# Kernel optimization log

Hardware: AMD Instinct MI355X
Metric: run time of the kernel (lower is better)

The kernel has to match this reference:

```python
import jax, jax.numpy as jnp
import numpy as np

N, E, F_IN, H0, H1, H2 = 50000, 800000, 128, 256, 256, 256
NEG = jnp.finfo(jnp.float32).min


def sage_max(x, src, dst, Wl, bl, Wr):
    # PyG SAGEConv(aggr='max'): lin_l(max_j x_j) + lin_r(x_i)
    agg = jax.ops.segment_max(x[src], dst, num_segments=N)  # [N, F]
    agg = jnp.where(agg <= NEG, 0.0, agg)  # isolated nodes -> 0
    return agg @ Wl + bl + x @ Wr


def setup_inputs() -> dict:
    key = jax.random.key(0)
    ks = jax.random.split(key, 16)
    g = lambda k, shp, fan: jax.random.normal(k, shp, jnp.float32) / np.sqrt(fan)
    inp = {
        "x": jax.random.normal(ks[0], (N, F_IN), jnp.float32),
        "edge_index": jax.random.randint(ks[1], (2, E), 0, N, jnp.int64),
        # shared_l1
        "Wl1": g(ks[2], (F_IN, H0), F_IN), "bl1": jnp.zeros((H0,), jnp.float32), "Wr1": g(ks[3], (F_IN, H0), F_IN),
        # shared_l2
        "Wl2": g(ks[4], (H0, H1), H0), "bl2": jnp.zeros((H1,), jnp.float32), "Wr2": g(ks[5], (H0, H1), H0),
        # rtang_l1 + head
        "Wla": g(ks[6], (H1, H2), H1), "bla": jnp.zeros((H2,), jnp.float32), "Wra": g(ks[7], (H1, H2), H1),
        "Wa": g(ks[8], (H2, 1), H2), "ba": jnp.zeros((1,), jnp.float32),
        # movedis_l1 + head
        "Wlm": g(ks[9], (H1, H2), H1), "blm": jnp.zeros((H2,), jnp.float32), "Wrm": g(ks[10], (H1, H2), H1),
        "Wm": g(ks[11], (H2, 1), H2), "bm": jnp.zeros((1,), jnp.float32),
    }
    return inp


def reference(x, edge_index, Wl1, bl1, Wr1, Wl2, bl2, Wr2,
              Wla, bla, Wra, Wa, ba, Wlm, blm, Wrm, Wm, bm):
    src, dst = edge_index[0], edge_index[1]
    h = jax.nn.relu(sage_max(x, src, dst, Wl1, bl1, Wr1))
    h = jax.nn.relu(sage_max(h, src, dst, Wl2, bl2, Wr2))
    rt = jax.nn.relu(sage_max(h, src, dst, Wla, bla, Wra))
    rt = (rt @ Wa + ba).reshape(-1)  # [N]
    mv = jax.nn.relu(sage_max(h, src, dst, Wlm, blm, Wrm))
    mv = (mv @ Wm + bm).reshape(-1)  # [N]
    return (rt, mv)
```

## Files before the change

### kernel.cpp

```cpp
#include <hip/hip_runtime.h>
#include <hip/hip_bf16.h>


#define NN 50000
#define NE 800000
#define HD 256
#define CAP 64

using bf16 = __hip_bfloat16;
typedef float f32x4 __attribute__((ext_vector_type(4)));
typedef short bf16x8 __attribute__((ext_vector_type(8)));

__device__ __forceinline__ void async16(const void* g, void* l) {
    __builtin_amdgcn_global_load_lds(
        (const __attribute__((address_space(1))) unsigned int*)g,
        (__attribute__((address_space(3))) unsigned int*)l, 16, 0, 0);
}

__device__ __forceinline__ unsigned short f2b(float f) {
    bf16 b = __float2bfloat16(f);
    return __builtin_bit_cast(unsigned short, b);
}

__global__ void k_scatter(const int* __restrict__ ei, int* __restrict__ cnt,
                          int* __restrict__ srcp) {
    int e = blockIdx.x * 256 + threadIdx.x;
    if (e < NE) {
        int d = ei[NE + e];
        int slot = atomicAdd(&cnt[d], 1);
        if (slot < CAP) srcp[(d << 6) + slot] = ei[e];
    }
}

__device__ __forceinline__ void pack1(const float* __restrict__ W,
                                      bf16* __restrict__ bt, int idx, int Ktot,
                                      int kofs) {
    int k = idx >> 8, n = idx & 255;
    bt[(size_t)n * Ktot + kofs + k] = __float2bfloat16(W[idx]);
}

#define PREP_CVT_B 6250
#define PREP_PACK_B 1792
#define PREP_CNT_B 196
#define PREP_B (PREP_CVT_B + PREP_PACK_B + PREP_CNT_B)

__global__ void k_prep(const float* __restrict__ x, bf16* __restrict__ xb,
                       const float* __restrict__ Wl1,
                       const float* __restrict__ Wr1,
                       const float* __restrict__ Wl2,
                       const float* __restrict__ Wr2,
                       const float* __restrict__ Wla,
                       const float* __restrict__ Wra,
                       const float* __restrict__ Wlm,
                       const float* __restrict__ Wrm, bf16* __restrict__ Bt1,
                       bf16* __restrict__ Bt2, bf16* __restrict__ Bta,
                       bf16* __restrict__ Btm, int* __restrict__ cnt) {
    int b = blockIdx.x;
    if (b < PREP_CVT_B) {
        int i = b * 256 + threadIdx.x;
        float4 v = ((const float4*)x)[i];
        ushort4 o;
        o.x = f2b(v.x); o.y = f2b(v.y); o.z = f2b(v.z); o.w = f2b(v.w);
        ((ushort4*)xb)[i] = o;
    } else if (b < PREP_CVT_B + PREP_PACK_B) {
        int idx = (b - PREP_CVT_B) * 256 + threadIdx.x;
        if (idx < 32768) pack1(Wl1, Bt1, idx, 256, 0);
        else if (idx < 65536) pack1(Wr1, Bt1, idx - 32768, 256, 128);
        else if (idx < 131072) pack1(Wl2, Bt2, idx - 65536, 512, 0);
        else if (idx < 196608) pack1(Wr2, Bt2, idx - 131072, 512, 256);
        else if (idx < 262144) pack1(Wla, Bta, idx - 196608, 512, 0);
        else if (idx < 327680) pack1(Wra, Bta, idx - 262144, 512, 256);
        else if (idx < 393216) pack1(Wlm, Btm, idx - 327680, 512, 0);
        else pack1(Wrm, Btm, idx - 393216, 512, 256);
    } else {
        int i = (b - PREP_CVT_B - PREP_PACK_B) * 256 + threadIdx.x;
        if (i < NN) cnt[i] = 0;
    }
}

template <int EPL>
__global__ __launch_bounds__(256) void k_agg(const bf16* __restrict__ feat,
                                             bf16* __restrict__ agg,
                                             const int* __restrict__ cnt,
                                             const int* __restrict__ srcp) {
    int node = blockIdx.x * 4 + (threadIdx.x >> 6);
    if (node >= NN) return;
    int lane = threadIdx.x & 63;
    int n = min(cnt[node], CAP);
    const int* __restrict__ lst = srcp + (node << 6);
    float m[EPL];
#pragma unroll
    for (int i = 0; i < EPL; ++i) m[i] = __int_as_float(0xff800000);

    auto acc2 = [&](unsigned v, int i0) {
        m[i0] = fmaxf(m[i0], __uint_as_float(v << 16));
        m[i0 + 1] = fmaxf(m[i0 + 1], __uint_as_float(v & 0xffff0000u));
    };

    int e = 0;
    for (; e + 3 < n; e += 4) {
        int sa = lst[e], sb = lst[e + 1], sc = lst[e + 2], sd = lst[e + 3];
        if (EPL == 2) {
            unsigned va = ((const unsigned*)feat)[(size_t)sa * 64 + lane];
            unsigned vb = ((const unsigned*)feat)[(size_t)sb * 64 + lane];
            unsigned vc = ((const unsigned*)feat)[(size_t)sc * 64 + lane];
            unsigned vd = ((const unsigned*)feat)[(size_t)sd * 64 + lane];
            acc2(va, 0); acc2(vb, 0); acc2(vc, 0); acc2(vd, 0);
        } else {
            uint2 va = ((const uint2*)feat)[(size_t)sa * 64 + lane];
            uint2 vb = ((const uint2*)feat)[(size_t)sb * 64 + lane];
            uint2 vc = ((const uint2*)feat)[(size_t)sc * 64 + lane];
            uint2 vd = ((const uint2*)feat)[(size_t)sd * 64 + lane];
            acc2(va.x, 0); acc2(va.y, 2);
            acc2(vb.x, 0); acc2(vb.y, 2);
            acc2(vc.x, 0); acc2(vc.y, 2);
            acc2(vd.x, 0); acc2(vd.y, 2);
        }
    }
    for (; e < n; ++e) {
        int s = lst[e];
        if (EPL == 2) {
            acc2(((const unsigned*)feat)[(size_t)s * 64 + lane], 0);
        } else {
            uint2 v = ((const uint2*)feat)[(size_t)s * 64 + lane];
            acc2(v.x, 0); acc2(v.y, 2);
        }
    }
    unsigned r0 = 0, r1 = 0;
    if (n > 0) {
        r0 = (__float_as_uint(m[0]) >> 16) | (__float_as_uint(m[1]) & 0xffff0000u);
        if (EPL == 4)
            r1 = (__float_as_uint(m[2]) >> 16) | (__float_as_uint(m[3]) & 0xffff0000u);
    }
    if (EPL == 2) {
        ((unsigned*)agg)[(size_t)node * 64 + lane] = r0;
    } else {
        ((uint2*)agg)[(size_t)node * 64 + lane] = make_uint2(r0, r1);
    }
}

__device__ __forceinline__ void gemm_core256(const bf16* __restrict__ A0,
                                             const bf16* __restrict__ A1, int F,
                                             int Ktot,
                                             const bf16* __restrict__ Bt,
                                             int bm0, int t, short* As,
                                             short* Bs, f32x4 (&acc)[4][8]) {
    const int wave = t >> 6;
    const int lane = t & 63;
    const int q = lane >> 4;
    const int c = lane & 15;
    const int wr = (wave >> 1) * 64;
    const int wcl = (wave & 1) * 128;

    for (int k0 = 0; k0 < Ktot; k0 += 64) {
        const bf16* Asrc = (k0 < F) ? A0 : A1;
        const int kk = (k0 < F) ? k0 : k0 - F;
        __syncthreads();
#pragma unroll
        for (int it = 0; it < 4; ++it) {
            int chunk = it * 256 + t;
            int row = chunk >> 3, kc = chunk & 7;
            int kcg = kc ^ (row & 7);
            int grow = bm0 + row;
            if (grow > NN - 1) grow = NN - 1;
            async16(Asrc + (size_t)grow * F + kk + kcg * 8, &As[chunk * 8]);
        }
#pragma unroll
        for (int it = 0; it < 8; ++it) {
            int chunk = it * 256 + t;
            int row = chunk >> 3, kc = chunk & 7;
            int kcg = kc ^ (row & 7);
            async16(Bt + (size_t)row * Ktot + k0 + kcg * 8, &Bs[chunk * 8]);
        }
        __syncthreads();
#pragma unroll
        for (int ks = 0; ks < 2; ++ks) {
            bf16x8 af[4], bfr[8];
            int ch = (ks * 4 + q) ^ (c & 7);
#pragma unroll
            for (int i = 0; i < 4; ++i)
                af[i] = *(const bf16x8*)&As[(wr + i * 16 + c) * 64 + ch * 8];
#pragma unroll
            for (int j = 0; j < 8; ++j)
                bfr[j] = *(const bf16x8*)&Bs[(wcl + j * 16 + c) * 64 + ch * 8];
#pragma unroll
            for (int i = 0; i < 4; ++i)
#pragma unroll
                for (int j = 0; j < 8; ++j)
                    acc[i][j] = __builtin_amdgcn_mfma_f32_16x16x32_bf16(
                        af[i], bfr[j], acc[i][j], 0, 0, 0);
        }
    }
}

__global__ __launch_bounds__(256, 2) void k_gemm_h(
    const bf16* __restrict__ A0, const bf16* __restrict__ A1, int F, int Ktot,
    const bf16* __restrict__ Bt, const float* __restrict__ bias,
    bf16* __restrict__ Hout) {
    __shared__ __attribute__((aligned(16))) short As[128 * 64];
    __shared__ __attribute__((aligned(16))) short Bs[256 * 64];
    const int t = threadIdx.x;
    const int bm0 = blockIdx.x * 128;
    const int wave = t >> 6;
    const int lane = t & 63;
    const int q = lane >> 4;
    const int c = lane & 15;
    const int wr = (wave >> 1) * 64;
    const int wcl = (wave & 1) * 128;

    f32x4 acc[4][8];
#pragma unroll
    for (int i = 0; i < 4; ++i)
#pragma unroll
        for (int j = 0; j < 8; ++j) acc[i][j] = (f32x4){0.f, 0.f, 0.f, 0.f};
    gemm_core256(A0, A1, F, Ktot, Bt, bm0, t, As, Bs, acc);

    float bcol[8];
#pragma unroll
    for (int j = 0; j < 8; ++j) bcol[j] = bias[wcl + j * 16 + c];
#pragma unroll
    for (int i = 0; i < 4; ++i)
#pragma unroll
        for (int r = 0; r < 4; ++r) {
            int row = bm0 + wr + i * 16 + q * 4 + r;
            if (row < NN) {
#pragma unroll
                for (int j = 0; j < 8; ++j) {
                    int col = wcl + j * 16 + c;
                    float v = fmaxf(acc[i][j][r] + bcol[j], 0.f);
                    Hout[(size_t)row * HD + col] = __float2bfloat16(v);
                }
            }
        }
}

__global__ __launch_bounds__(256, 2) void k_gemm_heads(
    const bf16* __restrict__ A0, const bf16* __restrict__ A1,
    const bf16* __restrict__ Bta, const float* __restrict__ bla,
    const float* __restrict__ Wa, const float* __restrict__ ba,
    const bf16* __restrict__ Btm, const float* __restrict__ blm,
    const float* __restrict__ Wm, const float* __restrict__ bm,
    float* __restrict__ out) {
    __shared__ __attribute__((aligned(16))) short As[128 * 64];
    __shared__ __attribute__((aligned(16))) short Bs[256 * 64];
    const int t = threadIdx.x;
    const int bm0 = blockIdx.x * 128;
    const int z = blockIdx.y;
    const bf16* Bt = z ? Btm : Bta;
    const float* bias = z ? blm : bla;
    const float* Wh = z ? Wm : Wa;
    const float hb = z ? bm[0] : ba[0];
    float* outp = out + (size_t)z * NN;
    const int wave = t >> 6;
    const int lane = t & 63;
    const int q = lane >> 4;
    const int c = lane & 15;
    const int wr = (wave >> 1) * 64;
    const int wcl = (wave & 1) * 128;

    f32x4 acc[4][8];
#pragma unroll
    for (int i = 0; i < 4; ++i)
#pragma unroll
        for (int j = 0; j < 8; ++j) acc[i][j] = (f32x4){0.f, 0.f, 0.f, 0.f};
    gemm_core256(A0, A1, 256, 512, Bt, bm0, t, As, Bs, acc);

    float bcol[8], wcol[8];
#pragma unroll
    for (int j = 0; j < 8; ++j) {
        int col = wcl + j * 16 + c;
        bcol[j] = bias[col];
        wcol[j] = Wh[col];
    }
    float pr[4][4];
#pragma unroll
    for (int i = 0; i < 4; ++i)
#pragma unroll
        for (int r = 0; r < 4; ++r) {
            float p = 0.f;
#pragma unroll
            for (int j = 0; j < 8; ++j)
                p += fmaxf(acc[i][j][r] + bcol[j], 0.f) * wcol[j];
            p += __shfl_xor(p, 1, 64);
            p += __shfl_xor(p, 2, 64);
            p += __shfl_xor(p, 4, 64);
            p += __shfl_xor(p, 8, 64);
            pr[i][r] = p;
        }
    __syncthreads();
    float* red = (float*)As;
    if ((wave & 1) && c == 0) {
#pragma unroll
        for (int i = 0; i < 4; ++i)
#pragma unroll
            for (int r = 0; r < 4; ++r) red[wr + i * 16 + q * 4 + r] = pr[i][r];
    }
    __syncthreads();
    if (!(wave & 1) && c == 0) {
#pragma unroll
        for (int i = 0; i < 4; ++i)
#pragma unroll
            for (int r = 0; r < 4; ++r) {
                int lr = wr + i * 16 + q * 4 + r;
                int row = bm0 + lr;
                if (row < NN) outp[row] = pr[i][r] + red[lr] + hb;
            }
    }
}

extern "C" void kernel_launch(void* const* d_in, const int* in_sizes, int n_in,
                              void* d_out, int out_size, void* d_ws,
                              size_t ws_size, hipStream_t stream) {
    const float* x = (const float*)d_in[0];
    const int* ei = (const int*)d_in[1];
    const float* Wl1 = (const float*)d_in[2];
    const float* bl1 = (const float*)d_in[3];
    const float* Wr1 = (const float*)d_in[4];
    const float* Wl2 = (const float*)d_in[5];
    const float* bl2 = (const float*)d_in[6];
    const float* Wr2 = (const float*)d_in[7];
    const float* Wla = (const float*)d_in[8];
    const float* bla = (const float*)d_in[9];
    const float* Wra = (const float*)d_in[10];
    const float* Wa = (const float*)d_in[11];
    const float* ba = (const float*)d_in[12];
    const float* Wlm = (const float*)d_in[13];
    const float* blm = (const float*)d_in[14];
    const float* Wrm = (const float*)d_in[15];
    const float* Wm = (const float*)d_in[16];
    const float* bm = (const float*)d_in[17];
    float* out = (float*)d_out;

    char* ws = (char*)d_ws;
    size_t off = 0;
    auto alloc = [&](size_t b) {
        void* p = ws + off;
        off = (off + b + 255) & ~(size_t)255;
        return p;
    };
    int* srcp = (int*)alloc((size_t)NN * CAP * 4);
    int* cnt = (int*)alloc((size_t)NN * 4);
    bf16* xb = (bf16*)alloc((size_t)NN * 128 * 2);
    bf16* h1 = (bf16*)alloc((size_t)NN * 256 * 2);
    bf16* h2 = (bf16*)alloc((size_t)NN * 256 * 2);
    bf16* agg = (bf16*)alloc((size_t)NN * 256 * 2);
    bf16* Bt1 = (bf16*)alloc((size_t)256 * 256 * 2);
    bf16* Bt2 = (bf16*)alloc((size_t)256 * 512 * 2);
    bf16* Bta = (bf16*)alloc((size_t)256 * 512 * 2);
    bf16* Btm = (bf16*)alloc((size_t)256 * 512 * 2);
    (void)ws_size; (void)in_sizes; (void)n_in; (void)out_size;

    k_prep<<<PREP_B, 256, 0, stream>>>(x, xb, Wl1, Wr1, Wl2, Wr2, Wla, Wra,
                                       Wlm, Wrm, Bt1, Bt2, Bta, Btm, cnt);
    k_scatter<<<(NE + 255) / 256, 256, 0, stream>>>(ei, cnt, srcp);

    const int GB = (NN + 127) / 128;
    k_agg<2><<<(NN + 3) / 4, 256, 0, stream>>>(xb, agg, cnt, srcp);
    k_gemm_h<<<GB, 256, 0, stream>>>(agg, xb, 128, 256, Bt1, bl1, h1);
    k_agg<4><<<(NN + 3) / 4, 256, 0, stream>>>(h1, agg, cnt, srcp);
    k_gemm_h<<<GB, 256, 0, stream>>>(agg, h1, 256, 512, Bt2, bl2, h2);
    k_agg<4><<<(NN + 3) / 4, 256, 0, stream>>>(h2, agg, cnt, srcp);
    dim3 gh(GB, 2);
    k_gemm_heads<<<gh, 256, 0, stream>>>(agg, h2, Bta, bla, Wa, ba, Btm, blm,
                                         Wm, bm, out);
}
```

Baseline: 369.1 us.

## Split max-aggregation into feature slices with edge-parallel lane groups

```diff
diff --git a/kernel.cpp b/kernel.cpp
--- a/kernel.cpp
+++ b/kernel.cpp
@@ -78,64 +78,49 @@
     }
 }
 
-template <int EPL>
-__global__ __launch_bounds__(256) void k_agg(const bf16* __restrict__ feat,
-                                             bf16* __restrict__ agg,
-                                             const int* __restrict__ cnt,
-                                             const int* __restrict__ srcp) {
-    int node = blockIdx.x * 4 + (threadIdx.x >> 6);
+template <int NSLICE>
+__global__ __launch_bounds__(256) void k_agg_sl(const bf16* __restrict__ feat,
+                                                bf16* __restrict__ agg,
+                                                const int* __restrict__ cnt,
+                                                const int* __restrict__ srcp) {
+    const int FU = NSLICE * 16;
+    int b = blockIdx.x;
+    int slice = b & (NSLICE - 1);
+    int node = (b / NSLICE) * 4 + (threadIdx.x >> 6);
     if (node >= NN) return;
     int lane = threadIdx.x & 63;
+    int g = lane >> 4, cc = lane & 15;
     int n = min(cnt[node], CAP);
     const int* __restrict__ lst = srcp + (node << 6);
-    float m[EPL];
-#pragma unroll
-    for (int i = 0; i < EPL; ++i) m[i] = __int_as_float(0xff800000);
-
-    auto acc2 = [&](unsigned v, int i0) {
-        m[i0] = fmaxf(m[i0], __uint_as_float(v << 16));
-        m[i0 + 1] = fmaxf(m[i0 + 1], __uint_as_float(v & 0xffff0000u));
-    };
-
-    int e = 0;
-    for (; e + 3 < n; e += 4) {
-        int sa = lst[e], sb = lst[e + 1], sc = lst[e + 2], sd = lst[e + 3];
-        if (EPL == 2) {
-            unsigned va = ((const unsigned*)feat)[(size_t)sa * 64 + lane];
-            unsigned vb = ((const unsigned*)feat)[(size_t)sb * 64 + lane];
-            unsigned vc = ((const unsigned*)feat)[(size_t)sc * 64 + lane];
-            unsigned vd = ((const unsigned*)feat)[(size_t)sd * 64 + lane];
-            acc2(va, 0); acc2(vb, 0); acc2(vc, 0); acc2(vd, 0);
-        } else {
-            uint2 va = ((const uint2*)feat)[(size_t)sa * 64 + lane];
-            uint2 vb = ((const uint2*)feat)[(size_t)sb * 64 + lane];
-            uint2 vc = ((const uint2*)feat)[(size_t)sc * 64 + lane];
-            uint2 vd = ((const uint2*)feat)[(size_t)sd * 64 + lane];
-            acc2(va.x, 0); acc2(va.y, 2);
-            acc2(vb.x, 0); acc2(vb.y, 2);
-            acc2(vc.x, 0); acc2(vc.y, 2);
-            acc2(vd.x, 0); acc2(vd.y, 2);
-        }
-    }
-    for (; e < n; ++e) {
+    const unsigned* __restrict__ fp = (const unsigned*)feat + slice * 16 + cc;
+
+    float m0 = __int_as_float(0xff800000), m1 = m0;
+    int e = g;
+    for (; e + 4 < n; e += 8) {
+        int sa = lst[e], sb = lst[e + 4];
+        unsigned va = fp[(size_t)sa * FU];
+        unsigned vb = fp[(size_t)sb * FU];
+        m0 = fmaxf(m0, __uint_as_float(va << 16));
+        m1 = fmaxf(m1, __uint_as_float(va & 0xffff0000u));
+        m0 = fmaxf(m0, __uint_as_float(vb << 16));
+        m1 = fmaxf(m1, __uint_as_float(vb & 0xffff0000u));
+    }
+    if (e < n) {
         int s = lst[e];
-        if (EPL == 2) {
-            acc2(((const unsigned*)feat)[(size_t)s * 64 + lane], 0);
-        } else {
-            uint2 v = ((const uint2*)feat)[(size_t)s * 64 + lane];
-            acc2(v.x, 0); acc2(v.y, 2);
-        }
-    }
-    unsigned r0 = 0, r1 = 0;
-    if (n > 0) {
-        r0 = (__float_as_uint(m[0]) >> 16) | (__float_as_uint(m[1]) & 0xffff0000u);
-        if (EPL == 4)
-            r1 = (__float_as_uint(m[2]) >> 16) | (__float_as_uint(m[3]) & 0xffff0000u);
-    }
-    if (EPL == 2) {
-        ((unsigned*)agg)[(size_t)node * 64 + lane] = r0;
-    } else {
-        ((uint2*)agg)[(size_t)node * 64 + lane] = make_uint2(r0, r1);
+        unsigned v = fp[(size_t)s * FU];
+        m0 = fmaxf(m0, __uint_as_float(v << 16));
+        m1 = fmaxf(m1, __uint_as_float(v & 0xffff0000u));
+    }
+    m0 = fmaxf(m0, __shfl_xor(m0, 16, 64));
+    m0 = fmaxf(m0, __shfl_xor(m0, 32, 64));
+    m1 = fmaxf(m1, __shfl_xor(m1, 16, 64));
+    m1 = fmaxf(m1, __shfl_xor(m1, 32, 64));
+    if (g == 0) {
+        unsigned r = 0;
+        if (n > 0)
+            r = (__float_as_uint(m0) >> 16) |
+                (__float_as_uint(m1) & 0xffff0000u);
+        ((unsigned*)agg)[(size_t)node * FU + slice * 16 + cc] = r;
     }
 }
 
@@ -355,11 +340,12 @@
     k_scatter<<<(NE + 255) / 256, 256, 0, stream>>>(ei, cnt, srcp);
 
     const int GB = (NN + 127) / 128;
-    k_agg<2><<<(NN + 3) / 4, 256, 0, stream>>>(xb, agg, cnt, srcp);
+    const int NG4 = (NN + 3) / 4;
+    k_agg_sl<4><<<NG4 * 4, 256, 0, stream>>>(xb, agg, cnt, srcp);
     k_gemm_h<<<GB, 256, 0, stream>>>(agg, xb, 128, 256, Bt1, bl1, h1);
-    k_agg<4><<<(NN + 3) / 4, 256, 0, stream>>>(h1, agg, cnt, srcp);
+    k_agg_sl<8><<<NG4 * 8, 256, 0, stream>>>(h1, agg, cnt, srcp);
     k_gemm_h<<<GB, 256, 0, stream>>>(agg, h1, 256, 512, Bt2, bl2, h2);
-    k_agg<4><<<(NN + 3) / 4, 256, 0, stream>>>(h2, agg, cnt, srcp);
+    k_agg_sl<8><<<NG4 * 8, 256, 0, stream>>>(h2, agg, cnt, srcp);
     dim3 gh(GB, 2);
     k_gemm_heads<<<gh, 256, 0, stream>>>(agg, h2, Bta, bla, Wa, ba, Btm, blm,
                                          Wm, bm, out);
```

Measured after the change: 581.1 us. 1.57x slower.

## Fuse all stages into one cooperative persistent kernel with grid syncs

Applied to the files above, without the earlier changes.

```diff
diff --git a/kernel.cpp b/kernel.cpp
--- a/kernel.cpp
+++ b/kernel.cpp
@@ -1,15 +1,31 @@
 #include <hip/hip_runtime.h>
 #include <hip/hip_bf16.h>
+#include <hip/hip_cooperative_groups.h>
 
 
 #define NN 50000
 #define NE 800000
 #define HD 256
 #define CAP 64
+#define FGRID 512
 
 using bf16 = __hip_bfloat16;
 typedef float f32x4 __attribute__((ext_vector_type(4)));
 typedef short bf16x8 __attribute__((ext_vector_type(8)));
+namespace cg = cooperative_groups;
+
+struct KParams {
+    const float* x; const int* ei;
+    const float* Wl1; const float* bl1; const float* Wr1;
+    const float* Wl2; const float* bl2; const float* Wr2;
+    const float* Wla; const float* bla; const float* Wra;
+    const float* Wa;  const float* ba;
+    const float* Wlm; const float* blm; const float* Wrm;
+    const float* Wm;  const float* bm;
+    float* out;
+    int* srcp; int* cnt;
+    bf16 *xb, *h1, *h2, *agg, *Bt1, *Bt2, *Bta, *Btm;
+};
 
 __device__ __forceinline__ void async16(const void* g, void* l) {
     __builtin_amdgcn_global_load_lds(
@@ -20,16 +36,6 @@
 __device__ __forceinline__ unsigned short f2b(float f) {
     bf16 b = __float2bfloat16(f);
     return __builtin_bit_cast(unsigned short, b);
-}
-
-__global__ void k_scatter(const int* __restrict__ ei, int* __restrict__ cnt,
-                          int* __restrict__ srcp) {
-    int e = blockIdx.x * 256 + threadIdx.x;
-    if (e < NE) {
-        int d = ei[NE + e];
-        int slot = atomicAdd(&cnt[d], 1);
-        if (slot < CAP) srcp[(d << 6) + slot] = ei[e];
-    }
 }
 
 __device__ __forceinline__ void pack1(const float* __restrict__ W,
@@ -43,49 +49,51 @@
 #define PREP_PACK_B 1792
 #define PREP_CNT_B 196
 #define PREP_B (PREP_CVT_B + PREP_PACK_B + PREP_CNT_B)
-
-__global__ void k_prep(const float* __restrict__ x, bf16* __restrict__ xb,
-                       const float* __restrict__ Wl1,
-                       const float* __restrict__ Wr1,
-                       const float* __restrict__ Wl2,
-                       const float* __restrict__ Wr2,
-                       const float* __restrict__ Wla,
-                       const float* __restrict__ Wra,
-                       const float* __restrict__ Wlm,
-                       const float* __restrict__ Wrm, bf16* __restrict__ Bt1,
-                       bf16* __restrict__ Bt2, bf16* __restrict__ Bta,
-                       bf16* __restrict__ Btm, int* __restrict__ cnt) {
-    int b = blockIdx.x;
+#define SCAT_B ((NE + 255) / 256)
+#define NG4 ((NN + 3) / 4)
+#define GB ((NN + 127) / 128)
+
+__device__ __forceinline__ void prep_body(int b, int t, const KParams& p) {
     if (b < PREP_CVT_B) {
-        int i = b * 256 + threadIdx.x;
-        float4 v = ((const float4*)x)[i];
+        int i = b * 256 + t;
+        float4 v = ((const float4*)p.x)[i];
         ushort4 o;
         o.x = f2b(v.x); o.y = f2b(v.y); o.z = f2b(v.z); o.w = f2b(v.w);
-        ((ushort4*)xb)[i] = o;
+        ((ushort4*)p.xb)[i] = o;
     } else if (b < PREP_CVT_B + PREP_PACK_B) {
-        int idx = (b - PREP_CVT_B) * 256 + threadIdx.x;
-        if (idx < 32768) pack1(Wl1, Bt1, idx, 256, 0);
-        else if (idx < 65536) pack1(Wr1, Bt1, idx - 32768, 256, 128);
-        else if (idx < 131072) pack1(Wl2, Bt2, idx - 65536, 512, 0);
-        else if (idx < 196608) pack1(Wr2, Bt2, idx - 131072, 512, 256);
-        else if (idx < 262144) pack1(Wla, Bta, idx - 196608, 512, 0);
-        else if (idx < 327680) pack1(Wra, Bta, idx - 262144, 512, 256);
-        else if (idx < 393216) pack1(Wlm, Btm, idx - 327680, 512, 0);
-        else pack1(Wrm, Btm, idx - 393216, 512, 256);
+        int idx = (b - PREP_CVT_B) * 256 + t;
+        if (idx < 32768) pack1(p.Wl1, p.Bt1, idx, 256, 0);
+        else if (idx < 65536) pack1(p.Wr1, p.Bt1, idx - 32768, 256, 128);
+        else if (idx < 131072) pack1(p.Wl2, p.Bt2, idx - 65536, 512, 0);
+        else if (idx < 196608) pack1(p.Wr2, p.Bt2, idx - 131072, 512, 256);
+        else if (idx < 262144) pack1(p.Wla, p.Bta, idx - 196608, 512, 0);
+        else if (idx < 327680) pack1(p.Wra, p.Bta, idx - 262144, 512, 256);
+        else if (idx < 393216) pack1(p.Wlm, p.Btm, idx - 327680, 512, 0);
+        else pack1(p.Wrm, p.Btm, idx - 393216, 512, 256);
     } else {
-        int i = (b - PREP_CVT_B - PREP_PACK_B) * 256 + threadIdx.x;
-        if (i < NN) cnt[i] = 0;
+        int i = (b - PREP_CVT_B - PREP_PACK_B) * 256 + t;
+        if (i < NN) p.cnt[i] = 0;
+    }
+}
+
+__device__ __forceinline__ void scatter_body(int b, int t, const KParams& p) {
+    int e = b * 256 + t;
+    if (e < NE) {
+        int d = p.ei[NE + e];
+        int slot = atomicAdd(&p.cnt[d], 1);
+        if (slot < CAP) p.srcp[(d << 6) + slot] = p.ei[e];
     }
 }
 
 template <int EPL>
-__global__ __launch_bounds__(256) void k_agg(const bf16* __restrict__ feat,
-                                             bf16* __restrict__ agg,
-                                             const int* __restrict__ cnt,
-                                             const int* __restrict__ srcp) {
-    int node = blockIdx.x * 4 + (threadIdx.x >> 6);
+__device__ __forceinline__ void agg_body(int vb, int t,
+                                         const bf16* __restrict__ feat,
+                                         bf16* __restrict__ agg,
+                                         const int* __restrict__ cnt,
+                                         const int* __restrict__ srcp) {
+    int node = vb * 4 + (t >> 6);
     if (node >= NN) return;
-    int lane = threadIdx.x & 63;
+    int lane = t & 63;
     int n = min(cnt[node], CAP);
     const int* __restrict__ lst = srcp + (node << 6);
     float m[EPL];
@@ -98,23 +106,44 @@
     };
 
     int e = 0;
+    for (; e + 7 < n; e += 8) {
+        int s[8];
+#pragma unroll
+        for (int j = 0; j < 8; ++j) s[j] = lst[e + j];
+        if (EPL == 2) {
+            unsigned v[8];
+#pragma unroll
+            for (int j = 0; j < 8; ++j)
+                v[j] = ((const unsigned*)feat)[(size_t)s[j] * 64 + lane];
+#pragma unroll
+            for (int j = 0; j < 8; ++j) acc2(v[j], 0);
+        } else {
+            uint2 v[8];
+#pragma unroll
+            for (int j = 0; j < 8; ++j)
+                v[j] = ((const uint2*)feat)[(size_t)s[j] * 64 + lane];
+#pragma unroll
+            for (int j = 0; j < 8; ++j) { acc2(v[j].x, 0); acc2(v[j].y, 2); }
+        }
+    }
     for (; e + 3 < n; e += 4) {
-        int sa = lst[e], sb = lst[e + 1], sc = lst[e + 2], sd = lst[e + 3];
+        int s[4];
+#pragma unroll
+        for (int j = 0; j < 4; ++j) s[j] = lst[e + j];
         if (EPL == 2) {
-            unsigned va = ((const unsigned*)feat)[(size_t)sa * 64 + lane];
-            unsigned vb = ((const unsigned*)feat)[(size_t)sb * 64 + lane];
-            unsigned vc = ((const unsigned*)feat)[(size_t)sc * 64 + lane];
-            unsigned vd = ((const unsigned*)feat)[(size_t)sd * 64 + lane];
-            acc2(va, 0); acc2(vb, 0); acc2(vc, 0); acc2(vd, 0);
+            unsigned v[4];
+#pragma unroll
+            for (int j = 0; j < 4; ++j)
+                v[j] = ((const unsigned*)feat)[(size_t)s[j] * 64 + lane];
+#pragma unroll
+            for (int j = 0; j < 4; ++j) acc2(v[j], 0);
         } else {
-            uint2 va = ((const uint2*)feat)[(size_t)sa * 64 + lane];
-            uint2 vb = ((const uint2*)feat)[(size_t)sb * 64 + lane];
-            uint2 vc = ((const uint2*)feat)[(size_t)sc * 64 + lane];
-            uint2 vd = ((const uint2*)feat)[(size_t)sd * 64 + lane];
-            acc2(va.x, 0); acc2(va.y, 2);
-            acc2(vb.x, 0); acc2(vb.y, 2);
-            acc2(vc.x, 0); acc2(vc.y, 2);
-            acc2(vd.x, 0); acc2(vd.y, 2);
+            uint2 v[4];
+#pragma unroll
+            for (int j = 0; j < 4; ++j)
+                v[j] = ((const uint2*)feat)[(size_t)s[j] * 64 + lane];
+#pragma unroll
+            for (int j = 0; j < 4; ++j) { acc2(v[j].x, 0); acc2(v[j].y, 2); }
         }
     }
     for (; e < n; ++e) {
@@ -193,14 +222,15 @@
     }
 }
 
-__global__ __launch_bounds__(256, 2) void k_gemm_h(
-    const bf16* __restrict__ A0, const bf16* __restrict__ A1, int F, int Ktot,
-    const bf16* __restrict__ Bt, const float* __restrict__ bias,
-    bf16* __restrict__ Hout) {
-    __shared__ __attribute__((aligned(16))) short As[128 * 64];
-    __shared__ __attribute__((aligned(16))) short Bs[256 * 64];
-    const int t = threadIdx.x;
-    const int bm0 = blockIdx.x * 128;
+__device__ __forceinline__ void gemm_h_body(int tile, int t,
+                                            const bf16* __restrict__ A0,
+                                            const bf16* __restrict__ A1, int F,
+                                            int Ktot,
+                                            const bf16* __restrict__ Bt,
+                                            const float* __restrict__ bias,
+                                            bf16* __restrict__ Hout, short* As,
+                                            short* Bs) {
+    const int bm0 = tile * 128;
     const int wave = t >> 6;
     const int lane = t & 63;
     const int q = lane >> 4;
@@ -234,23 +264,15 @@
         }
 }
 
-__global__ __launch_bounds__(256, 2) void k_gemm_heads(
-    const bf16* __restrict__ A0, const bf16* __restrict__ A1,
-    const bf16* __restrict__ Bta, const float* __restrict__ bla,
-    const float* __restrict__ Wa, const float* __restrict__ ba,
-    const bf16* __restrict__ Btm, const float* __restrict__ blm,
-    const float* __restrict__ Wm, const float* __restrict__ bm,
-    float* __restrict__ out) {
-    __shared__ __attribute__((aligned(16))) short As[128 * 64];
-    __shared__ __attribute__((aligned(16))) short Bs[256 * 64];
-    const int t = threadIdx.x;
-    const int bm0 = blockIdx.x * 128;
-    const int z = blockIdx.y;
-    const bf16* Bt = z ? Btm : Bta;
-    const float* bias = z ? blm : bla;
-    const float* Wh = z ? Wm : Wa;
-    const float hb = z ? bm[0] : ba[0];
-    float* outp = out + (size_t)z * NN;
+__device__ __forceinline__ void heads_body(int vb, int t, const KParams& p,
+                                           short* As, short* Bs) {
+    const int z = (vb >= GB) ? 1 : 0;
+    const int bm0 = (vb - z * GB) * 128;
+    const bf16* Bt = z ? p.Btm : p.Bta;
+    const float* bias = z ? p.blm : p.bla;
+    const float* Wh = z ? p.Wm : p.Wa;
+    const float hb = z ? p.bm[0] : p.ba[0];
+    float* outp = p.out + (size_t)z * NN;
     const int wave = t >> 6;
     const int lane = t & 63;
     const int q = lane >> 4;
@@ -263,7 +285,7 @@
     for (int i = 0; i < 4; ++i)
 #pragma unroll
         for (int j = 0; j < 8; ++j) acc[i][j] = (f32x4){0.f, 0.f, 0.f, 0.f};
-    gemm_core256(A0, A1, 256, 512, Bt, bm0, t, As, Bs, acc);
+    gemm_core256(p.agg, p.h2, 256, 512, Bt, bm0, t, As, Bs, acc);
 
     float bcol[8], wcol[8];
 #pragma unroll
@@ -277,15 +299,15 @@
     for (int i = 0; i < 4; ++i)
 #pragma unroll
         for (int r = 0; r < 4; ++r) {
-            float p = 0.f;
+            float pv = 0.f;
 #pragma unroll
             for (int j = 0; j < 8; ++j)
-                p += fmaxf(acc[i][j][r] + bcol[j], 0.f) * wcol[j];
-            p += __shfl_xor(p, 1, 64);
-            p += __shfl_xor(p, 2, 64);
-            p += __shfl_xor(p, 4, 64);
-            p += __shfl_xor(p, 8, 64);
-            pr[i][r] = p;
+                pv += fmaxf(acc[i][j][r] + bcol[j], 0.f) * wcol[j];
+            pv += __shfl_xor(pv, 1, 64);
+            pv += __shfl_xor(pv, 2, 64);
+            pv += __shfl_xor(pv, 4, 64);
+            pv += __shfl_xor(pv, 8, 64);
+            pr[i][r] = pv;
         }
     __syncthreads();
     float* red = (float*)As;
@@ -308,59 +330,110 @@
     }
 }
 
+__global__ __launch_bounds__(256, 2) void k_fused(KParams p) {
+    __shared__ __attribute__((aligned(16))) short As[128 * 64];
+    __shared__ __attribute__((aligned(16))) short Bs[256 * 64];
+    cg::grid_group grid = cg::this_grid();
+    const int t = threadIdx.x;
+    const int gsz = gridDim.x;
+
+    for (int vb = blockIdx.x; vb < PREP_B; vb += gsz) prep_body(vb, t, p);
+    grid.sync();
+    for (int vb = blockIdx.x; vb < SCAT_B; vb += gsz) scatter_body(vb, t, p);
+    grid.sync();
+    for (int vb = blockIdx.x; vb < NG4; vb += gsz)
+        agg_body<2>(vb, t, p.xb, p.agg, p.cnt, p.srcp);
+    grid.sync();
+    for (int vb = blockIdx.x; vb < GB; vb += gsz)
+        gemm_h_body(vb, t, p.agg, p.xb, 128, 256, p.Bt1, p.bl1, p.h1, As, Bs);
+    grid.sync();
+    for (int vb = blockIdx.x; vb < NG4; vb += gsz)
+        agg_body<4>(vb, t, p.h1, p.agg, p.cnt, p.srcp);
+    grid.sync();
+    for (int vb = blockIdx.x; vb < GB; vb += gsz)
+        gemm_h_body(vb, t, p.agg, p.h1, 256, 512, p.Bt2, p.bl2, p.h2, As, Bs);
+    grid.sync();
+    for (int vb = blockIdx.x; vb < NG4; vb += gsz)
+        agg_body<4>(vb, t, p.h2, p.agg, p.cnt, p.srcp);
+    grid.sync();
+    for (int vb = blockIdx.x; vb < 2 * GB; vb += gsz) heads_body(vb, t, p, As, Bs);
+}
+
+__global__ __launch_bounds__(256) void kw_prep(KParams p) {
+    prep_body(blockIdx.x, threadIdx.x, p);
+}
+__global__ __launch_bounds__(256) void kw_scatter(KParams p) {
+    scatter_body(blockIdx.x, threadIdx.x, p);
+}
+template <int EPL>
+__global__ __launch_bounds__(256) void kw_agg(KParams p, const bf16* feat) {
+    agg_body<EPL>(blockIdx.x, threadIdx.x, feat, p.agg, p.cnt, p.srcp);
+}
+__global__ __launch_bounds__(256, 2) void kw_gemm_h(const bf16* A0,
+                                                    const bf16* A1, int F,
+                                                    int Ktot, const bf16* Bt,
+                                                    const float* bias,
+                                                    bf16* Hout) {
+    __shared__ __attribute__((aligned(16))) short As[128 * 64];
+    __shared__ __attribute__((aligned(16))) short Bs[256 * 64];
+    gemm_h_body(blockIdx.x, threadIdx.x, A0, A1, F, Ktot, Bt, bias, Hout, As,
+                Bs);
+}
+__global__ __launch_bounds__(256, 2) void kw_heads(KParams p) {
+    __shared__ __attribute__((aligned(16))) short As[128 * 64];
+    __shared__ __attribute__((aligned(16))) short Bs[256 * 64];
+    heads_body(blockIdx.x, threadIdx.x, p, As, Bs);
+}
+
 extern "C" void kernel_launch(void* const* d_in, const int* in_sizes, int n_in,
                               void* d_out, int out_size, void* d_ws,
                               size_t ws_size, hipStream_t stream) {
-    const float* x = (const float*)d_in[0];
-    const int* ei = (const int*)d_in[1];
-    const float* Wl1 = (const float*)d_in[2];
-    const float* bl1 = (const float*)d_in[3];
-    const float* Wr1 = (const float*)d_in[4];
-    const float* Wl2 = (const float*)d_in[5];
-    const float* bl2 = (const float*)d_in[6];
-    const float* Wr2 = (const float*)d_in[7];
-    const float* Wla = (const float*)d_in[8];
-    const float* bla = (const float*)d_in[9];
-    const float* Wra = (const float*)d_in[10];
-    const float* Wa = (const float*)d_in[11];
-    const float* ba = (const float*)d_in[12];
-    const float* Wlm = (const float*)d_in[13];
-    const float* blm = (const float*)d_in[14];
-    const float* Wrm = (const float*)d_in[15];
-    const float* Wm = (const float*)d_in[16];
-    const float* bm = (const float*)d_in[17];
-    float* out = (float*)d_out;
-
     char* ws = (char*)d_ws;
     size_t off = 0;
     auto alloc = [&](size_t b) {
-        void* p = ws + off;
+        void* pp = ws + off;
         off = (off + b + 255) & ~(size_t)255;
-        return p;
+        return pp;
     };
-    int* srcp = (int*)alloc((size_t)NN * CAP * 4);
-    int* cnt = (int*)alloc((size_t)NN * 4);
-    bf16* xb = (bf16*)alloc((size_t)NN * 128 * 2);
-    bf16* h1 = (bf16*)alloc((size_t)NN * 256 * 2);
-    bf16* h2 = (bf16*)alloc((size_t)NN * 256 * 2);
-    bf16* agg = (bf16*)alloc((size_t)NN * 256 * 2);
-    bf16* Bt1 = (bf16*)alloc((size_t)256 * 256 * 2);
-    bf16* Bt2 = (bf16*)alloc((size_t)256 * 512 * 2);
-    bf16* Bta = (bf16*)alloc((size_t)256 * 512 * 2);
-    bf16* Btm = (bf16*)alloc((size_t)256 * 512 * 2);
+    KParams p;
+    p.x = (const float*)d_in[0];
+    p.ei = (const int*)d_in[1];
+    p.Wl1 = (const float*)d_in[2];  p.bl1 = (const float*)d_in[3];
+    p.Wr1 = (const float*)d_in[4];
+    p.Wl2 = (const float*)d_in[5];  p.bl2 = (const float*)d_in[6];
+    p.Wr2 = (const float*)d_in[7];
+    p.Wla = (const float*)d_in[8];  p.bla = (const float*)d_in[9];
+    p.Wra = (const float*)d_in[10];
+    p.Wa = (const float*)d_in[11];  p.ba = (const float*)d_in[12];
+    p.Wlm = (const float*)d_in[13]; p.blm = (const float*)d_in[14];
+    p.Wrm = (const float*)d_in[15];
+    p.Wm = (const float*)d_in[16];  p.bm = (const float*)d_in[17];
+    p.out = (float*)d_out;
+    p.srcp = (int*)alloc((size_t)NN * CAP * 4);
+    p.cnt = (int*)alloc((size_t)NN * 4);
+    p.xb = (bf16*)alloc((size_t)NN * 128 * 2);
+    p.h1 = (bf16*)alloc((size_t)NN * 256 * 2);
+    p.h2 = (bf16*)alloc((size_t)NN * 256 * 2);
+    p.agg = (bf16*)alloc((size_t)NN * 256 * 2);
+    p.Bt1 = (bf16*)alloc((size_t)256 * 256 * 2);
+    p.Bt2 = (bf16*)alloc((size_t)256 * 512 * 2);
+    p.Bta = (bf16*)alloc((size_t)256 * 512 * 2);
+    p.Btm = (bf16*)alloc((size_t)256 * 512 * 2);
     (void)ws_size; (void)in_sizes; (void)n_in; (void)out_size;
 
-    k_prep<<<PREP_B, 256, 0, stream>>>(x, xb, Wl1, Wr1, Wl2, Wr2, Wla, Wra,
-                                       Wlm, Wrm, Bt1, Bt2, Bta, Btm, cnt);
-    k_scatter<<<(NE + 255) / 256, 256, 0, stream>>>(ei, cnt, srcp);
-
-    const int GB = (NN + 127) / 128;
-    k_agg<2><<<(NN + 3) / 4, 256, 0, stream>>>(xb, agg, cnt, srcp);
-    k_gemm_h<<<GB, 256, 0, stream>>>(agg, xb, 128, 256, Bt1, bl1, h1);
-    k_agg<4><<<(NN + 3) / 4, 256, 0, stream>>>(h1, agg, cnt, srcp);
-    k_gemm_h<<<GB, 256, 0, stream>>>(agg, h1, 256, 512, Bt2, bl2, h2);
-    k_agg<4><<<(NN + 3) / 4, 256, 0, stream>>>(h2, agg, cnt, srcp);
-    dim3 gh(GB, 2);
-    k_gemm_heads<<<gh, 256, 0, stream>>>(agg, h2, Bta, bla, Wa, ba, Btm, blm,
-                                         Wm, bm, out);
-}
+    void* args[] = {&p};
+    hipError_t err = hipLaunchCooperativeKernel((void*)k_fused, dim3(FGRID),
+                                                dim3(256), args, 0, stream);
+    if (err != hipSuccess) {
+        kw_prep<<<PREP_B, 256, 0, stream>>>(p);
+        kw_scatter<<<SCAT_B, 256, 0, stream>>>(p);
+        kw_agg<2><<<NG4, 256, 0, stream>>>(p, p.xb);
+        kw_gemm_h<<<GB, 256, 0, stream>>>(p.agg, p.xb, 128, 256, p.Bt1, p.bl1,
+                                          p.h1);
+        kw_agg<4><<<NG4, 256, 0, stream>>>(p, p.h1);
+        kw_gemm_h<<<GB, 256, 0, stream>>>(p.agg, p.h1, 256, 512, p.Bt2, p.bl2,
+                                          p.h2);
+        kw_agg<4><<<NG4, 256, 0, stream>>>(p, p.h2);
+        kw_heads<<<2 * GB, 256, 0, stream>>>(p);
+    }
+}
```

New measurement: 937.2 us. 2.54x slower.
